# Kernel tuning notes

Hardware: AMD Instinct MI355X
Metric: run time of the kernel (lower is better)

Reference implementation:

```python
import jax, jax.numpy as jnp
import numpy as np

N_NODES = 40000
N_EDGES = 640000


def setup_inputs() -> dict:
    key = jax.random.key(0)
    ks = jax.random.split(key, 6)
    src_edges = jax.random.randint(ks[0], (N_EDGES,), 0, N_NODES, dtype=jnp.int32)
    dst_edges = jnp.sort(jax.random.randint(ks[1], (N_EDGES,), 0, N_NODES, dtype=jnp.int32))
    features = jax.random.normal(ks[2], (N_NODES, 128), dtype=jnp.float32)
    # GINConv.reset_parameters: uniform(-stdv, stdv), stdv = 1/sqrt(output_dim)
    def init_w(k, din, dout):
        stdv = 1.0 / np.sqrt(dout)
        return jax.random.uniform(k, (din, dout), jnp.float32, -stdv, stdv)
    W1 = init_w(ks[3], 128, 128)
    W2 = init_w(ks[4], 128, 128)
    W3 = init_w(ks[5], 128, 64)
    return {"src_edges": src_edges, "dst_edges": dst_edges, "features": features,
            "W1": W1, "W2": W2, "W3": W3}


def _gin_layer(h, src, dst, W):
    # gather src features [E, d], segment-sum into dst nodes, then linear
    agg = jax.ops.segment_sum(h[src], dst, num_segments=N_NODES)  # [N, d_in]
    return agg @ W  # [N, d_out]


def reference(src_edges, dst_edges, features, W1, W2, W3):
    src = src_edges.astype(jnp.int32)
    dst = dst_edges.astype(jnp.int32)
    h = _gin_layer(features, src, dst, W1)
    h = _gin_layer(h, src, dst, W2)  # dropout p=0.0 -> identity
    h = _gin_layer(h, src, dst, W3)
    return h
```

## Files before the change

### kernel.cpp

```cpp
#include <hip/hip_runtime.h>
#include <hip/hip_bf16.h>

#define N_NODES 40000
#define N_EDGES 640000

typedef __attribute__((ext_vector_type(8))) short bfrag;
typedef __attribute__((ext_vector_type(4))) float ffrag;

__device__ __forceinline__ float b2f_lo(unsigned u) {
    return __builtin_bit_cast(float, u << 16);
}
__device__ __forceinline__ float b2f_hi(unsigned u) {
    return __builtin_bit_cast(float, u & 0xffff0000u);
}
__device__ __forceinline__ unsigned short f2b(float f) {
    return __builtin_bit_cast(unsigned short, __float2bfloat16(f));
}

#define RP_BLOCKS 782
#define W_BLOCKS  32
__global__ __launch_bounds__(256) void prep(const int* __restrict__ dst,
                                            int* __restrict__ rowptr,
                                            const float* __restrict__ W1,
                                            const float* __restrict__ W2,
                                            const float* __restrict__ W3,
                                            unsigned short* __restrict__ Wt123) {
    __shared__ float uS[4][128];
    const int bid = blockIdx.x;
    if (bid < RP_BLOCKS) {
        int i = bid * 256 + threadIdx.x;
        if (i < N_EDGES / 4) {
            int e = i * 4;
            int4 d4 = *(const int4*)(dst + e);
            int dp = (e == 0) ? -1 : dst[e - 1];
            for (int n = dp + 1;   n <= d4.x; n++) rowptr[n] = e;
            for (int n = d4.x + 1; n <= d4.y; n++) rowptr[n] = e + 1;
            for (int n = d4.y + 1; n <= d4.z; n++) rowptr[n] = e + 2;
            for (int n = d4.z + 1; n <= d4.w; n++) rowptr[n] = e + 3;
        } else if (i < N_EDGES / 4 + N_NODES + 1) {
            int n = i - N_EDGES / 4;
            if (n > dst[N_EDGES - 1]) rowptr[n] = N_EDGES;
        }
        return;
    }

    const int wv   = threadIdx.x >> 6;
    const int lane = threadIdx.x & 63;
    const int k    = (bid - RP_BLOCKS) * 4 + wv;

    float u0 = 0.f, u1 = 0.f;
    const float* w1p = W1 + k * 128;
    const float* w2p = W2 + 2 * lane;
#pragma unroll 8
    for (int j = 0; j < 128; j++) {
        float a  = w1p[j];
        float2 w = *(const float2*)(w2p + (size_t)j * 128);
        u0 += a * w.x;
        u1 += a * w.y;
    }
    uS[wv][2 * lane]     = u0;
    uS[wv][2 * lane + 1] = u1;
    __syncthreads();

    float acc = 0.f;
    const float* w3p = W3 + lane;
#pragma unroll 8
    for (int l = 0; l < 128; l++)
        acc += uS[wv][l] * w3p[(size_t)l * 64];
    Wt123[lane * 128 + k] = f2b(acc);
}

__global__ __launch_bounds__(256) void gemm_mfma64(const float* __restrict__ X,
                                                   const unsigned short* __restrict__ Wt,
                                                   unsigned short* __restrict__ Y) {
    const int wv   = threadIdx.x >> 6;
    const int lane = threadIdx.x & 63;
    const int ml   = lane & 15;
    const int quad = lane >> 4;
    const int row0 = blockIdx.x * 64 + wv * 16;

    ffrag acc[4];
#pragma unroll
    for (int c = 0; c < 4; c++) acc[c] = (ffrag)0.f;

#pragma unroll
    for (int kb = 0; kb < 128; kb += 32) {
        const float* p = X + (size_t)(row0 + ml) * 128 + kb + quad * 8;
        float4 u0 = *(const float4*)p;
        float4 u1 = *(const float4*)(p + 4);
        bfrag a;
        a[0] = (short)f2b(u0.x); a[1] = (short)f2b(u0.y);
        a[2] = (short)f2b(u0.z); a[3] = (short)f2b(u0.w);
        a[4] = (short)f2b(u1.x); a[5] = (short)f2b(u1.y);
        a[6] = (short)f2b(u1.z); a[7] = (short)f2b(u1.w);
#pragma unroll
        for (int c = 0; c < 4; c++) {
            const int col = c * 16 + ml;
            bfrag b = *(const bfrag*)(Wt + (size_t)col * 128 + kb + quad * 8);
            acc[c] = __builtin_amdgcn_mfma_f32_16x16x32_bf16(a, b, acc[c], 0, 0, 0);
        }
    }
#pragma unroll
    for (int c = 0; c < 4; c++)
#pragma unroll
        for (int i = 0; i < 4; i++)
            Y[(size_t)(row0 + quad * 4 + i) * 64 + c * 16 + ml] = f2b(acc[c][i]);
}

template<bool OUT_F32>
__global__ __launch_bounds__(256) void scatter8(const unsigned short* __restrict__ T,
                                                const int* __restrict__ srcE,
                                                const int* __restrict__ rowptr,
                                                void* __restrict__ Hv) {
    const int wave = blockIdx.x * 4 + (threadIdx.x >> 6);
    const int lane = threadIdx.x & 63;
    const int g    = lane >> 3;
    const int c8   = (lane & 7) * 8;
    const int node = wave * 8 + g;
    if (node >= N_NODES) return;
    const int e0 = rowptr[node], e1 = rowptr[node + 1];

    float a0 = 0.f, a1 = 0.f, a2 = 0.f, a3 = 0.f;
    float a4 = 0.f, a5 = 0.f, a6 = 0.f, a7 = 0.f;

    int e = e0;
    uint4 t0, t1, t2, t3;
    bool have = (e + 4 <= e1);
    if (have) {
        int s0 = srcE[e], s1 = srcE[e + 1], s2 = srcE[e + 2], s3 = srcE[e + 3];
        t0 = *(const uint4*)(T + (size_t)s0 * 64 + c8);
        t1 = *(const uint4*)(T + (size_t)s1 * 64 + c8);
        t2 = *(const uint4*)(T + (size_t)s2 * 64 + c8);
        t3 = *(const uint4*)(T + (size_t)s3 * 64 + c8);
        e += 4;
    }
    while (have) {
        const bool next = (e + 4 <= e1);
        int s0, s1, s2, s3;
        if (next) {
            s0 = srcE[e]; s1 = srcE[e + 1]; s2 = srcE[e + 2]; s3 = srcE[e + 3];
        }
        a0 += (b2f_lo(t0.x) + b2f_lo(t1.x)) + (b2f_lo(t2.x) + b2f_lo(t3.x));
        a1 += (b2f_hi(t0.x) + b2f_hi(t1.x)) + (b2f_hi(t2.x) + b2f_hi(t3.x));
        a2 += (b2f_lo(t0.y) + b2f_lo(t1.y)) + (b2f_lo(t2.y) + b2f_lo(t3.y));
        a3 += (b2f_hi(t0.y) + b2f_hi(t1.y)) + (b2f_hi(t2.y) + b2f_hi(t3.y));
        a4 += (b2f_lo(t0.z) + b2f_lo(t1.z)) + (b2f_lo(t2.z) + b2f_lo(t3.z));
        a5 += (b2f_hi(t0.z) + b2f_hi(t1.z)) + (b2f_hi(t2.z) + b2f_hi(t3.z));
        a6 += (b2f_lo(t0.w) + b2f_lo(t1.w)) + (b2f_lo(t2.w) + b2f_lo(t3.w));
        a7 += (b2f_hi(t0.w) + b2f_hi(t1.w)) + (b2f_hi(t2.w) + b2f_hi(t3.w));
        if (next) {
            t0 = *(const uint4*)(T + (size_t)s0 * 64 + c8);
            t1 = *(const uint4*)(T + (size_t)s1 * 64 + c8);
            t2 = *(const uint4*)(T + (size_t)s2 * 64 + c8);
            t3 = *(const uint4*)(T + (size_t)s3 * 64 + c8);
            e += 4;
        }
        have = next;
    }

    const int rem = e1 - e;
    if (rem > 0) {
        int s0 = srcE[e];
        int s1 = (rem > 1) ? srcE[e + 1] : s0;
        int s2 = (rem > 2) ? srcE[e + 2] : s0;
        uint4 q0 = *(const uint4*)(T + (size_t)s0 * 64 + c8);
        uint4 q1 = *(const uint4*)(T + (size_t)s1 * 64 + c8);
        uint4 q2 = *(const uint4*)(T + (size_t)s2 * 64 + c8);
        a0 += b2f_lo(q0.x); a1 += b2f_hi(q0.x);
        a2 += b2f_lo(q0.y); a3 += b2f_hi(q0.y);
        a4 += b2f_lo(q0.z); a5 += b2f_hi(q0.z);
        a6 += b2f_lo(q0.w); a7 += b2f_hi(q0.w);
        if (rem > 1) {
            a0 += b2f_lo(q1.x); a1 += b2f_hi(q1.x);
            a2 += b2f_lo(q1.y); a3 += b2f_hi(q1.y);
            a4 += b2f_lo(q1.z); a5 += b2f_hi(q1.z);
            a6 += b2f_lo(q1.w); a7 += b2f_hi(q1.w);
        }
        if (rem > 2) {
            a0 += b2f_lo(q2.x); a1 += b2f_hi(q2.x);
            a2 += b2f_lo(q2.y); a3 += b2f_hi(q2.y);
            a4 += b2f_lo(q2.z); a5 += b2f_hi(q2.z);
            a6 += b2f_lo(q2.w); a7 += b2f_hi(q2.w);
        }
    }

    if constexpr (OUT_F32) {
        float* q = (float*)Hv + (size_t)node * 64 + c8;
        *(float4*)q       = make_float4(a0, a1, a2, a3);
        *(float4*)(q + 4) = make_float4(a4, a5, a6, a7);
    } else {
        ushort4 o0, o1;
        o0.x = f2b(a0); o0.y = f2b(a1); o0.z = f2b(a2); o0.w = f2b(a3);
        o1.x = f2b(a4); o1.y = f2b(a5); o1.z = f2b(a6); o1.w = f2b(a7);
        unsigned short* q = (unsigned short*)Hv + (size_t)node * 64 + c8;
        *(ushort4*)q       = o0;
        *(ushort4*)(q + 4) = o1;
    }
}

extern "C" void kernel_launch(void* const* d_in, const int* in_sizes, int n_in,
                              void* d_out, int out_size, void* d_ws, size_t ws_size,
                              hipStream_t stream) {
    const int*   src  = (const int*)d_in[0];
    const int*   dst  = (const int*)d_in[1];
    const float* feat = (const float*)d_in[2];
    const float* W1   = (const float*)d_in[3];
    const float* W2   = (const float*)d_in[4];
    const float* W3   = (const float*)d_in[5];
    float* out = (float*)d_out;

    char* wsb = (char*)d_ws;
    unsigned short* T     = (unsigned short*)wsb;
    unsigned short* H     = (unsigned short*)(wsb + (size_t)5505024);
    int* rowptr           = (int*)(wsb + (size_t)11010048);
    unsigned short* Wt123 = (unsigned short*)(wsb + (size_t)11010048 + 163968);

    const int scatterBlocks = (N_NODES + 31) / 32;

    prep<<<RP_BLOCKS + W_BLOCKS, 256, 0, stream>>>(dst, rowptr, W1, W2, W3, Wt123);
    gemm_mfma64<<<625, 256, 0, stream>>>(feat, Wt123, T);
    scatter8<false><<<scatterBlocks, 256, 0, stream>>>(T, src, rowptr, H);
    scatter8<false><<<scatterBlocks, 256, 0, stream>>>(H, src, rowptr, T);
    scatter8<true><<<scatterBlocks, 256, 0, stream>>>(T, src, rowptr, out);
}
```

Measured before the change: 134.4 us.

## Stage block edge indices in LDS and double-buffer gathers in scatter

Each 32-node block now cooperatively loads its contiguous range of source indices into shared memory, then each 8-lane group reads indices from LDS instead of global memory. The gather loop is double-buffered with two sets of four in-flight row loads, aiming to hide gather latency and shorten the dependent index-then-feature load chain. A fallback path keeps the old global-index loop when a block's edge count exceeds the LDS buffer. This adds a block barrier and LDS usage, which may reduce occupancy, and the removed node bounds check relies on the node count dividing evenly by 32.

```diff
diff --git a/kernel.cpp b/kernel.cpp
--- a/kernel.cpp
+++ b/kernel.cpp
@@ -107,82 +107,147 @@
             Y[(size_t)(row0 + quad * 4 + i) * 64 + c * 16 + ml] = f2b(acc[c][i]);
 }
 
+#define IDX_LDS 2048
 template<bool OUT_F32>
 __global__ __launch_bounds__(256) void scatter8(const unsigned short* __restrict__ T,
                                                 const int* __restrict__ srcE,
                                                 const int* __restrict__ rowptr,
                                                 void* __restrict__ Hv) {
-    const int wave = blockIdx.x * 4 + (threadIdx.x >> 6);
-    const int lane = threadIdx.x & 63;
+    __shared__ int shIdx[IDX_LDS];
+    const int tid   = threadIdx.x;
+    const int node0 = blockIdx.x * 32;
+    const int ebase = rowptr[node0];
+    const int etop  = rowptr[node0 + 32];
+    const int total = etop - ebase;
+
+    const int lim = total < IDX_LDS ? total : IDX_LDS;
+    for (int j = tid; j < lim; j += 256) shIdx[j] = srcE[ebase + j];
+    __syncthreads();
+
+    const int lane = tid & 63;
     const int g    = lane >> 3;
     const int c8   = (lane & 7) * 8;
-    const int node = wave * 8 + g;
-    if (node >= N_NODES) return;
+    const int node = node0 + (tid >> 6) * 8 + g;
     const int e0 = rowptr[node], e1 = rowptr[node + 1];
 
     float a0 = 0.f, a1 = 0.f, a2 = 0.f, a3 = 0.f;
     float a4 = 0.f, a5 = 0.f, a6 = 0.f, a7 = 0.f;
 
+#define GATH(s) (*(const uint4*)(T + (size_t)(s) * 64 + c8))
+#define ACCQ(t0, t1, t2, t3)                                                  \
+    do {                                                                      \
+        a0 += (b2f_lo(t0.x) + b2f_lo(t1.x)) + (b2f_lo(t2.x) + b2f_lo(t3.x));  \
+        a1 += (b2f_hi(t0.x) + b2f_hi(t1.x)) + (b2f_hi(t2.x) + b2f_hi(t3.x));  \
+        a2 += (b2f_lo(t0.y) + b2f_lo(t1.y)) + (b2f_lo(t2.y) + b2f_lo(t3.y));  \
+        a3 += (b2f_hi(t0.y) + b2f_hi(t1.y)) + (b2f_hi(t2.y) + b2f_hi(t3.y));  \
+        a4 += (b2f_lo(t0.z) + b2f_lo(t1.z)) + (b2f_lo(t2.z) + b2f_lo(t3.z));  \
+        a5 += (b2f_hi(t0.z) + b2f_hi(t1.z)) + (b2f_hi(t2.z) + b2f_hi(t3.z));  \
+        a6 += (b2f_lo(t0.w) + b2f_lo(t1.w)) + (b2f_lo(t2.w) + b2f_lo(t3.w));  \
+        a7 += (b2f_hi(t0.w) + b2f_hi(t1.w)) + (b2f_hi(t2.w) + b2f_hi(t3.w));  \
+    } while (0)
+
     int e = e0;
-    uint4 t0, t1, t2, t3;
-    bool have = (e + 4 <= e1);
-    if (have) {
-        int s0 = srcE[e], s1 = srcE[e + 1], s2 = srcE[e + 2], s3 = srcE[e + 3];
-        t0 = *(const uint4*)(T + (size_t)s0 * 64 + c8);
-        t1 = *(const uint4*)(T + (size_t)s1 * 64 + c8);
-        t2 = *(const uint4*)(T + (size_t)s2 * 64 + c8);
-        t3 = *(const uint4*)(T + (size_t)s3 * 64 + c8);
-        e += 4;
-    }
-    while (have) {
-        const bool next = (e + 4 <= e1);
-        int s0, s1, s2, s3;
-        if (next) {
-            s0 = srcE[e]; s1 = srcE[e + 1]; s2 = srcE[e + 2]; s3 = srcE[e + 3];
-        }
-        a0 += (b2f_lo(t0.x) + b2f_lo(t1.x)) + (b2f_lo(t2.x) + b2f_lo(t3.x));
-        a1 += (b2f_hi(t0.x) + b2f_hi(t1.x)) + (b2f_hi(t2.x) + b2f_hi(t3.x));
-        a2 += (b2f_lo(t0.y) + b2f_lo(t1.y)) + (b2f_lo(t2.y) + b2f_lo(t3.y));
-        a3 += (b2f_hi(t0.y) + b2f_hi(t1.y)) + (b2f_hi(t2.y) + b2f_hi(t3.y));
-        a4 += (b2f_lo(t0.z) + b2f_lo(t1.z)) + (b2f_lo(t2.z) + b2f_lo(t3.z));
-        a5 += (b2f_hi(t0.z) + b2f_hi(t1.z)) + (b2f_hi(t2.z) + b2f_hi(t3.z));
-        a6 += (b2f_lo(t0.w) + b2f_lo(t1.w)) + (b2f_lo(t2.w) + b2f_lo(t3.w));
-        a7 += (b2f_hi(t0.w) + b2f_hi(t1.w)) + (b2f_hi(t2.w) + b2f_hi(t3.w));
-        if (next) {
-            t0 = *(const uint4*)(T + (size_t)s0 * 64 + c8);
-            t1 = *(const uint4*)(T + (size_t)s1 * 64 + c8);
-            t2 = *(const uint4*)(T + (size_t)s2 * 64 + c8);
-            t3 = *(const uint4*)(T + (size_t)s3 * 64 + c8);
+    if (total <= IDX_LDS) {
+        uint4 A0, A1, A2, A3, B0, B1, B2, B3;
+        bool haveA = false, haveB = false;
+        if (e + 4 <= e1) {
+            int o = e - ebase;
+            A0 = GATH(shIdx[o]);     A1 = GATH(shIdx[o + 1]);
+            A2 = GATH(shIdx[o + 2]); A3 = GATH(shIdx[o + 3]);
+            e += 4; haveA = true;
+            if (e + 4 <= e1) {
+                o = e - ebase;
+                B0 = GATH(shIdx[o]);     B1 = GATH(shIdx[o + 1]);
+                B2 = GATH(shIdx[o + 2]); B3 = GATH(shIdx[o + 3]);
+                e += 4; haveB = true;
+            }
+        }
+        while (haveA) {
+            ACCQ(A0, A1, A2, A3);
+            if (e + 4 <= e1) {
+                int o = e - ebase;
+                A0 = GATH(shIdx[o]);     A1 = GATH(shIdx[o + 1]);
+                A2 = GATH(shIdx[o + 2]); A3 = GATH(shIdx[o + 3]);
+                e += 4;
+            } else haveA = false;
+            if (!haveB) break;
+            ACCQ(B0, B1, B2, B3);
+            if (e + 4 <= e1) {
+                int o = e - ebase;
+                B0 = GATH(shIdx[o]);     B1 = GATH(shIdx[o + 1]);
+                B2 = GATH(shIdx[o + 2]); B3 = GATH(shIdx[o + 3]);
+                e += 4;
+            } else haveB = false;
+        }
+        const int rem = e1 - e;
+        if (rem > 0) {
+            int o = e - ebase;
+            int s0 = shIdx[o];
+            int s1 = (rem > 1) ? shIdx[o + 1] : s0;
+            int s2 = (rem > 2) ? shIdx[o + 2] : s0;
+            uint4 q0 = GATH(s0), q1 = GATH(s1), q2 = GATH(s2);
+            a0 += b2f_lo(q0.x); a1 += b2f_hi(q0.x);
+            a2 += b2f_lo(q0.y); a3 += b2f_hi(q0.y);
+            a4 += b2f_lo(q0.z); a5 += b2f_hi(q0.z);
+            a6 += b2f_lo(q0.w); a7 += b2f_hi(q0.w);
+            if (rem > 1) {
+                a0 += b2f_lo(q1.x); a1 += b2f_hi(q1.x);
+                a2 += b2f_lo(q1.y); a3 += b2f_hi(q1.y);
+                a4 += b2f_lo(q1.z); a5 += b2f_hi(q1.z);
+                a6 += b2f_lo(q1.w); a7 += b2f_hi(q1.w);
+            }
+            if (rem > 2) {
+                a0 += b2f_lo(q2.x); a1 += b2f_hi(q2.x);
+                a2 += b2f_lo(q2.y); a3 += b2f_hi(q2.y);
+                a4 += b2f_lo(q2.z); a5 += b2f_hi(q2.z);
+                a6 += b2f_lo(q2.w); a7 += b2f_hi(q2.w);
+            }
+        }
+    } else {
+        uint4 t0, t1, t2, t3;
+        bool have = (e + 4 <= e1);
+        if (have) {
+            int s0 = srcE[e], s1 = srcE[e + 1], s2 = srcE[e + 2], s3 = srcE[e + 3];
+            t0 = GATH(s0); t1 = GATH(s1); t2 = GATH(s2); t3 = GATH(s3);
             e += 4;
         }
-        have = next;
-    }
-
-    const int rem = e1 - e;
-    if (rem > 0) {
-        int s0 = srcE[e];
-        int s1 = (rem > 1) ? srcE[e + 1] : s0;
-        int s2 = (rem > 2) ? srcE[e + 2] : s0;
-        uint4 q0 = *(const uint4*)(T + (size_t)s0 * 64 + c8);
-        uint4 q1 = *(const uint4*)(T + (size_t)s1 * 64 + c8);
-        uint4 q2 = *(const uint4*)(T + (size_t)s2 * 64 + c8);
-        a0 += b2f_lo(q0.x); a1 += b2f_hi(q0.x);
-        a2 += b2f_lo(q0.y); a3 += b2f_hi(q0.y);
-        a4 += b2f_lo(q0.z); a5 += b2f_hi(q0.z);
-        a6 += b2f_lo(q0.w); a7 += b2f_hi(q0.w);
-        if (rem > 1) {
-            a0 += b2f_lo(q1.x); a1 += b2f_hi(q1.x);
-            a2 += b2f_lo(q1.y); a3 += b2f_hi(q1.y);
-            a4 += b2f_lo(q1.z); a5 += b2f_hi(q1.z);
-            a6 += b2f_lo(q1.w); a7 += b2f_hi(q1.w);
-        }
-        if (rem > 2) {
-            a0 += b2f_lo(q2.x); a1 += b2f_hi(q2.x);
-            a2 += b2f_lo(q2.y); a3 += b2f_hi(q2.y);
-            a4 += b2f_lo(q2.z); a5 += b2f_hi(q2.z);
-            a6 += b2f_lo(q2.w); a7 += b2f_hi(q2.w);
-        }
-    }
+        while (have) {
+            const bool next = (e + 4 <= e1);
+            int s0, s1, s2, s3;
+            if (next) { s0 = srcE[e]; s1 = srcE[e + 1]; s2 = srcE[e + 2]; s3 = srcE[e + 3]; }
+            ACCQ(t0, t1, t2, t3);
+            if (next) {
+                t0 = GATH(s0); t1 = GATH(s1); t2 = GATH(s2); t3 = GATH(s3);
+                e += 4;
+            }
+            have = next;
+        }
+        const int rem = e1 - e;
+        if (rem > 0) {
+            int s0 = srcE[e];
+            int s1 = (rem > 1) ? srcE[e + 1] : s0;
+            int s2 = (rem > 2) ? srcE[e + 2] : s0;
+            uint4 q0 = GATH(s0), q1 = GATH(s1), q2 = GATH(s2);
+            a0 += b2f_lo(q0.x); a1 += b2f_hi(q0.x);
+            a2 += b2f_lo(q0.y); a3 += b2f_hi(q0.y);
+            a4 += b2f_lo(q0.z); a5 += b2f_hi(q0.z);
+            a6 += b2f_lo(q0.w); a7 += b2f_hi(q0.w);
+            if (rem > 1) {
+                a0 += b2f_lo(q1.x); a1 += b2f_hi(q1.x);
+                a2 += b2f_lo(q1.y); a3 += b2f_hi(q1.y);
+                a4 += b2f_lo(q1.z); a5 += b2f_hi(q1.z);
+                a6 += b2f_lo(q1.w); a7 += b2f_hi(q1.w);
+            }
+            if (rem > 2) {
+                a0 += b2f_lo(q2.x); a1 += b2f_hi(q2.x);
+                a2 += b2f_lo(q2.y); a3 += b2f_hi(q2.y);
+                a4 += b2f_lo(q2.z); a5 += b2f_hi(q2.z);
+                a6 += b2f_lo(q2.w); a7 += b2f_hi(q2.w);
+            }
+        }
+    }
+#undef GATH
+#undef ACCQ
 
     if constexpr (OUT_F32) {
         float* q = (float*)Hv + (size_t)node * 64 + c8;
```

Result: no change. 133.5 us, median of 2 (-0.7%).
